# Optimization experiments

Measured on AMD Instinct MI355X. Metric: run time of the kernel, lower is better.

Reference implementation:

```python
import jax, jax.numpy as jnp
import numpy as np

N_NODES = 100000
N_EDGES = 1600000
N_GRAPHS = 2048


def _gcn_conv(x, src, dst, W, b, n_nodes):
    # PyG GCNConv: add self-loops, symmetric norm D^-1/2 A D^-1/2, then linear.
    h = x @ W  # [N, H]
    loop = jnp.arange(n_nodes, dtype=src.dtype)
    s = jnp.concatenate([src, loop])
    d = jnp.concatenate([dst, loop])
    deg = jax.ops.segment_sum(jnp.ones_like(d, dtype=h.dtype), d, num_segments=n_nodes)
    dinv = jax.lax.rsqrt(jnp.maximum(deg, 1.0))
    norm = dinv[s] * dinv[d]  # [E+N]
    msg = h[s] * norm[:, None]  # gathered, normalized messages
    out = jax.ops.segment_sum(msg, d, num_segments=n_nodes)
    return out + b


def _mean_pool(x, batch, n_graphs):
    sums = jax.ops.segment_sum(x, batch, num_segments=n_graphs)
    cnt = jax.ops.segment_sum(jnp.ones((x.shape[0],), x.dtype), batch, num_segments=n_graphs)
    return sums / jnp.maximum(cnt, 1.0)[:, None]


def setup_inputs() -> dict:
    key = jax.random.key(0)
    ks = jax.random.split(key, 8)
    x = jax.random.normal(ks[0], (N_NODES, 128), dtype=jnp.float32)
    edge_index = jax.random.randint(ks[1], (2, N_EDGES), 0, N_NODES, dtype=jnp.int64)
    batch = jnp.sort(jax.random.randint(ks[2], (N_NODES,), 0, N_GRAPHS, dtype=jnp.int64))
    W1 = jax.random.normal(ks[3], (128, 256), dtype=jnp.float32) * 0.05
    b1 = jnp.zeros((256,), jnp.float32)
    W2 = jax.random.normal(ks[4], (256, 256), dtype=jnp.float32) * 0.05
    b2 = jnp.zeros((256,), jnp.float32)
    Wc = jax.random.normal(ks[5], (256, 64), dtype=jnp.float32) * 0.05
    bc = jnp.zeros((64,), jnp.float32)
    return {"x": x, "edge_index": edge_index, "batch": batch,
            "W1": W1, "b1": b1, "W2": W2, "b2": b2, "Wc": Wc, "bc": bc}


def reference(x, edge_index, batch, W1, b1, W2, b2, Wc, bc):
    src, dst = edge_index[0], edge_index[1]
    n = x.shape[0]
    h = jax.nn.relu(_gcn_conv(x, src, dst, W1, b1, n))
    h = jax.nn.relu(_gcn_conv(h, src, dst, W2, b2, n))
    g = _mean_pool(h, batch, N_GRAPHS)  # [G, h2]
    logits = g @ Wc + bc
    return jax.nn.log_softmax(logits, axis=1)
```

## Files before the change

### kernel.cpp

```cpp
#include <hip/hip_runtime.h>
#include <hip/hip_bf16.h>

#define N_NODES 100000
#define N_EDGES 1600000
#define N_GRAPHS 2048
#define F0 128
#define F1 256
#define NCLS 64

#define BSHIFT 9
#define BNODES 512
#define NB 196
#define EPB 4096
#define NCHUNK 391
#define FLATN (NB * NCHUNK)

typedef unsigned int uint32;
typedef unsigned short u16;
typedef u16 u16x8 __attribute__((ext_vector_type(8)));
typedef __bf16 bf16x8 __attribute__((ext_vector_type(8)));
typedef float f32x4 __attribute__((ext_vector_type(4)));

__device__ __forceinline__ float blo(uint32 v) { return __builtin_bit_cast(float, v << 16); }
__device__ __forceinline__ float bhi(uint32 v) { return __builtin_bit_cast(float, v & 0xffff0000u); }
__device__ __forceinline__ float b16f(u16 v) { return __builtin_bit_cast(float, (uint32)v << 16); }
__device__ __forceinline__ u16 f2bf(float f) {
    uint32 u = __builtin_bit_cast(uint32, f);
    u += 0x7fffu + ((u >> 16) & 1u);
    return (u16)(u >> 16);
}
__device__ __forceinline__ uint32 pack2(float a, float b) {
    return (uint32)f2bf(a) | ((uint32)f2bf(b) << 16);
}
__device__ __forceinline__ float ub0(uint32 u) { return (float)(u & 255u); }
__device__ __forceinline__ float ub1(uint32 u) { return (float)((u >> 8) & 255u); }
__device__ __forceinline__ float ub2(uint32 u) { return (float)((u >> 16) & 255u); }
__device__ __forceinline__ float ub3(uint32 u) { return (float)(u >> 24); }

#define GLOAD_LDS16(g, l)                                                                  \
    __builtin_amdgcn_global_load_lds((const __attribute__((address_space(1))) void*)(g),   \
                                     (__attribute__((address_space(3))) void*)(l), 16, 0, 0)

#define SCAN_B 1024

__global__ void scan_partial(const int* __restrict__ in, int n, int* __restrict__ bsum) {
    __shared__ int lds[SCAN_B];
    int i = blockIdx.x * SCAN_B + threadIdx.x;
    lds[threadIdx.x] = (i < n) ? in[i] : 0;
    __syncthreads();
    for (int s = SCAN_B / 2; s > 0; s >>= 1) {
        if (threadIdx.x < s) lds[threadIdx.x] += lds[threadIdx.x + s];
        __syncthreads();
    }
    if (threadIdx.x == 0) bsum[blockIdx.x] = lds[0];
}

__global__ void scan_final(const int* __restrict__ in, int n, const int* __restrict__ bsum,
                           int nb, int* __restrict__ out) {
    __shared__ int lds[SCAN_B];
    __shared__ int bpre[128];
    if (threadIdx.x < 128) bpre[threadIdx.x] = (threadIdx.x < nb) ? bsum[threadIdx.x] : 0;
    __syncthreads();
    for (int s = 1; s < 128; s <<= 1) {
        int v = (threadIdx.x < 128 && threadIdx.x >= s) ? bpre[threadIdx.x - s] : 0;
        __syncthreads();
        if (threadIdx.x < 128) bpre[threadIdx.x] += v;
        __syncthreads();
    }
    int base = (blockIdx.x > 0) ? bpre[blockIdx.x - 1] : 0;
    int i = blockIdx.x * SCAN_B + threadIdx.x;
    int v = (i < n) ? in[i] : 0;
    lds[threadIdx.x] = v;
    __syncthreads();
    for (int s = 1; s < SCAN_B; s <<= 1) {
        int t = (threadIdx.x >= s) ? lds[threadIdx.x - s] : 0;
        __syncthreads();
        lds[threadIdx.x] += t;
        __syncthreads();
    }
    if (i < n) out[i + 1] = lds[threadIdx.x] + base;
    if (i == 0) out[0] = 0;
}


__global__ __launch_bounds__(256) void hist_pass(const int* __restrict__ dst,
                                                 int* __restrict__ hist) {
    __shared__ int lh[NB];
    int t = threadIdx.x, blk = blockIdx.x;
    if (t < NB) lh[t] = 0;
    __syncthreads();
#pragma unroll
    for (int k = 0; k < EPB / 256; ++k) {
        int e = blk * EPB + k * 256 + t;
        if (e < N_EDGES) atomicAdd(&lh[dst[e] >> BSHIFT], 1);
    }
    __syncthreads();
    if (t < NB) hist[t * NCHUNK + blk] = lh[t];
}

__global__ __launch_bounds__(256) void bin_pairs(const int* __restrict__ src,
                                                 const int* __restrict__ dst,
                                                 const int* __restrict__ histoff,
                                                 uint32* __restrict__ pairs) {
    __shared__ int lbase[NB];
    __shared__ int lcur[NB];
    int t = threadIdx.x, blk = blockIdx.x;
    if (t < NB) {
        lbase[t] = histoff[t * NCHUNK + blk];
        lcur[t] = 0;
    }
    __syncthreads();
#pragma unroll
    for (int k = 0; k < EPB / 256; ++k) {
        int e = blk * EPB + k * 256 + t;
        if (e < N_EDGES) {
            int d = dst[e], s = src[e];
            int b = d >> BSHIFT;
            int r = atomicAdd(&lcur[b], 1);
            pairs[lbase[b] + r] = (uint32)(d & (BNODES - 1)) | ((uint32)s << BSHIFT);
        }
    }
}

#define PCAP 16384

__global__ __launch_bounds__(256) void bucket_csr(const uint32* __restrict__ pairs,
                                                  const int* __restrict__ histoff,
                                                  int* __restrict__ offs,
                                                  int* __restrict__ csr,
                                                  float* __restrict__ dinv) {
    __shared__ uint32 lp[PCAP];
    __shared__ int lcnt[BNODES];
    __shared__ int lcur[BNODES];
    __shared__ int psum[256];
    int t = threadIdx.x, b = blockIdx.x;
    int n0 = b << BSHIFT;
    int nn = min(BNODES, N_NODES - n0);
    lcnt[t] = 0;
    lcnt[t + 256] = 0;
    __syncthreads();
    int ebase = histoff[b * NCHUNK];
    int eend = (b == NB - 1) ? N_EDGES : histoff[(b + 1) * NCHUNK];
    for (int i = ebase + t; i < eend; i += 256) {
        uint32 p = pairs[i];
        int li = i - ebase;
        if (li < PCAP) lp[li] = p;
        atomicAdd(&lcnt[p & (BNODES - 1)], 1);
    }
    __syncthreads();
    int c0 = lcnt[2 * t], c1 = lcnt[2 * t + 1];
    if (2 * t < nn) dinv[n0 + 2 * t] = rsqrtf((float)(c0 + 1));
    if (2 * t + 1 < nn) dinv[n0 + 2 * t + 1] = rsqrtf((float)(c1 + 1));
    psum[t] = c0 + c1;
    __syncthreads();
    for (int s = 1; s < 256; s <<= 1) {
        int v = (t >= s) ? psum[t - s] : 0;
        __syncthreads();
        psum[t] += v;
        __syncthreads();
    }
    int ep = psum[t] - (c0 + c1);
    lcur[2 * t] = ep;
    lcur[2 * t + 1] = ep + c0;
    if (2 * t < nn) offs[n0 + 2 * t] = ebase + ep;
    if (2 * t + 1 < nn) offs[n0 + 2 * t + 1] = ebase + ep + c0;
    if (b == NB - 1 && t == 0) offs[N_NODES] = N_EDGES;
    __syncthreads();
    for (int i = ebase + t; i < eend; i += 256) {
        int li = i - ebase;
        uint32 p = (li < PCAP) ? lp[li] : pairs[i];
        int r = atomicAdd(&lcur[p & (BNODES - 1)], 1);
        csr[ebase + r] = (int)(p >> BSHIFT);
    }
}


__global__ __launch_bounds__(256) void cast_q8_x(const float* __restrict__ x,
                                                 const float* __restrict__ dinv,
                                                 const int* __restrict__ batch,
                                                 u16* __restrict__ q8,
                                                 float* __restrict__ qs,
                                                 int* __restrict__ gcnt) {
    int node = blockIdx.x * 4 + (threadIdx.x >> 6);
    if (node >= N_NODES) return;
    int lane = threadIdx.x & 63;
    float d = dinv[node];
    float2 v = *(const float2*)&x[(size_t)node * F0 + lane * 2];
    float f0 = v.x * d, f1 = v.y * d;
    float m = fmaxf(fabsf(f0), fabsf(f1));
    for (int s = 32; s > 0; s >>= 1) m = fmaxf(m, __shfl_xor(m, s, 64));
    float inv = (m > 0.f) ? 127.f / m : 0.f;
    int u0 = (int)rintf(f0 * inv) + 128, u1 = (int)rintf(f1 * inv) + 128;
    q8[(size_t)node * 64 + lane] = (u16)((u0 & 255) | ((u1 & 255) << 8));
    if (lane == 0) {
        qs[node] = m * (1.f / 127.f);
        atomicAdd(&gcnt[batch[node]], 1);
    }
}


__global__ void transpose_w2(const float* __restrict__ W1, const float* __restrict__ W2,
                             u16* __restrict__ W1t, u16* __restrict__ W2t) {
    int id = blockIdx.x * blockDim.x + threadIdx.x;
    if (id < F0 * F1) {
        int k = id / F1, n = id % F1;
        W1t[(size_t)n * F0 + k] = f2bf(W1[id]);
    } else {
        int id2 = id - F0 * F1;
        if (id2 < F1 * F1) {
            int k = id2 / F1, n = id2 % F1;
            W2t[(size_t)n * F1 + k] = f2bf(W2[id2]);
        }
    }
}


template <int F>
__global__ __launch_bounds__(256) void aggregate_q8(const void* __restrict__ q8,
                                                    const float* __restrict__ qs,
                                                    const int* __restrict__ offs,
                                                    const int* __restrict__ csr,
                                                    const float* __restrict__ dinv,
                                                    u16* __restrict__ out) {
    constexpr int V = F / 64;
    int node = blockIdx.x * 4 + (threadIdx.x >> 6);
    if (node >= N_NODES) return;
    int lane = threadIdx.x & 63;
    float acc[V];
    float ssum;
    {
        float s = qs[node];
        ssum = s;
        if constexpr (V == 2) {
            uint32 q = (uint32)((const u16*)q8)[(size_t)node * 64 + lane];
            acc[0] = ub0(q) * s;
            acc[1] = ub1(q) * s;
        } else {
            uint32 q = ((const uint32*)q8)[(size_t)node * 64 + lane];
            acc[0] = ub0(q) * s;
            acc[1] = ub1(q) * s;
            acc[2] = ub2(q) * s;
            acc[3] = ub3(q) * s;
        }
    }
    int e0 = offs[node], e1 = offs[node + 1];
    for (int b = e0; b < e1; b += 64) {
        bool valid = (b + lane) < e1;
        int idx = valid ? csr[b + lane] : 0;
        float sv = valid ? qs[idx] : 0.f;
        int cnt = min(64, e1 - b);
        int t = 0;
        for (; t + 4 <= cnt; t += 4) {
            int j0 = __shfl(idx, t), j1 = __shfl(idx, t + 1);
            int j2 = __shfl(idx, t + 2), j3 = __shfl(idx, t + 3);
            float s0 = __shfl(sv, t), s1 = __shfl(sv, t + 1);
            float s2 = __shfl(sv, t + 2), s3 = __shfl(sv, t + 3);
            ssum += (s0 + s1) + (s2 + s3);
            if constexpr (V == 2) {
                uint32 a = (uint32)((const u16*)q8)[(size_t)j0 * 64 + lane];
                uint32 c = (uint32)((const u16*)q8)[(size_t)j1 * 64 + lane];
                uint32 d = (uint32)((const u16*)q8)[(size_t)j2 * 64 + lane];
                uint32 f = (uint32)((const u16*)q8)[(size_t)j3 * 64 + lane];
                acc[0] += ub0(a) * s0 + ub0(c) * s1 + ub0(d) * s2 + ub0(f) * s3;
                acc[1] += ub1(a) * s0 + ub1(c) * s1 + ub1(d) * s2 + ub1(f) * s3;
            } else {
                uint32 a = ((const uint32*)q8)[(size_t)j0 * 64 + lane];
                uint32 c = ((const uint32*)q8)[(size_t)j1 * 64 + lane];
                uint32 d = ((const uint32*)q8)[(size_t)j2 * 64 + lane];
                uint32 f = ((const uint32*)q8)[(size_t)j3 * 64 + lane];
                acc[0] += ub0(a) * s0 + ub0(c) * s1 + ub0(d) * s2 + ub0(f) * s3;
                acc[1] += ub1(a) * s0 + ub1(c) * s1 + ub1(d) * s2 + ub1(f) * s3;
                acc[2] += ub2(a) * s0 + ub2(c) * s1 + ub2(d) * s2 + ub2(f) * s3;
                acc[3] += ub3(a) * s0 + ub3(c) * s1 + ub3(d) * s2 + ub3(f) * s3;
            }
        }
        for (; t < cnt; ++t) {
            int j0 = __shfl(idx, t);
            float s0 = __shfl(sv, t);
            ssum += s0;
            if constexpr (V == 2) {
                uint32 a = (uint32)((const u16*)q8)[(size_t)j0 * 64 + lane];
                acc[0] += ub0(a) * s0;
                acc[1] += ub1(a) * s0;
            } else {
                uint32 a = ((const uint32*)q8)[(size_t)j0 * 64 + lane];
                acc[0] += ub0(a) * s0;
                acc[1] += ub1(a) * s0;
                acc[2] += ub2(a) * s0;
                acc[3] += ub3(a) * s0;
            }
        }
    }
    float di = dinv[node];
    float bias = 128.f * ssum;
    u16* orow = out + (size_t)node * F + lane * V;
    if constexpr (V == 2) {
        *(uint32*)orow = pack2((acc[0] - bias) * di, (acc[1] - bias) * di);
    } else {
        uint2 o;
        o.x = pack2((acc[0] - bias) * di, (acc[1] - bias) * di);
        o.y = pack2((acc[2] - bias) * di, (acc[3] - bias) * di);
        *(uint2*)orow = o;
    }
}


template <int K, bool QUANT>
__global__ __launch_bounds__(256) void gemm_fused(const u16* __restrict__ A,
                                                  const u16* __restrict__ Bt,
                                                  const float* __restrict__ bias,
                                                  const float* __restrict__ dinv,
                                                  int M,
                                                  uint32* __restrict__ q8,
                                                  float* __restrict__ qs,
                                                  const int* __restrict__ batch,
                                                  float* __restrict__ gpool) {
    constexpr int BM = 64, BN = 256, BK = 64;
    __shared__ __align__(16) char smem[40960];
    u16* As = (u16*)smem;
    u16* Bs = (u16*)smem + BM * BK;
    int tid = threadIdx.x;
    int lane = tid & 63;
    int wid = __builtin_amdgcn_readfirstlane(tid >> 6);
    int row0 = blockIdx.x * BM;
    int lr = lane & 15, lq = lane >> 4;
    int wn = wid * 64;
    int srow = lane >> 3;
    int schunk = (lane & 7) * 8;

    f32x4 acc[4][4];
#pragma unroll
    for (int i = 0; i < 4; ++i)
#pragma unroll
        for (int j = 0; j < 4; ++j) acc[i][j] = (f32x4){0.f, 0.f, 0.f, 0.f};

    for (int k0 = 0; k0 < K; k0 += BK) {
#pragma unroll
        for (int p = 0; p < 2; ++p) {
            int r0 = wid * 16 + p * 8;
            const u16* g = A + (size_t)(row0 + r0 + srow) * K + k0 + schunk;
            GLOAD_LDS16(g, As + r0 * BK);
        }
#pragma unroll
        for (int p = 0; p < 8; ++p) {
            int r0 = wid * 64 + p * 8;
            const u16* g = Bt + (size_t)(r0 + srow) * K + k0 + schunk;
            GLOAD_LDS16(g, Bs + r0 * BK);
        }
        __syncthreads();
#pragma unroll
        for (int kk = 0; kk < BK; kk += 32) {
            bf16x8 af[4], bfr[4];
#pragma unroll
            for (int i = 0; i < 4; ++i)
                af[i] = __builtin_bit_cast(bf16x8, *(const u16x8*)&As[(i * 16 + lr) * BK + kk + lq * 8]);
#pragma unroll
            for (int j = 0; j < 4; ++j)
                bfr[j] = __builtin_bit_cast(bf16x8, *(const u16x8*)&Bs[(wn + j * 16 + lr) * BK + kk + lq * 8]);
#pragma unroll
            for (int i = 0; i < 4; ++i)
#pragma unroll
                for (int j = 0; j < 4; ++j)
                    acc[i][j] = __builtin_amdgcn_mfma_f32_16x16x32_bf16(af[i], bfr[j], acc[i][j], 0, 0, 0);
        }
        __syncthreads();
    }

    u16(*P)[260] = (u16(*)[260])smem;
#pragma unroll
    for (int i = 0; i < 4; ++i) {
#pragma unroll
        for (int j = 0; j < 4; ++j) {
            int cl = wn + j * 16 + lr;
            float bv = bias[cl];
#pragma unroll
            for (int r = 0; r < 4; ++r) {
                int rl = i * 16 + lq * 4 + r;
                int row = row0 + rl;
                float v = 0.f;
                if (row < M) {
                    v = fmaxf(acc[i][j][r] + bv, 0.f);
                    if constexpr (QUANT) v *= dinv[row];
                }
                P[rl][cl] = f2bf(v);
            }
        }
    }

    if constexpr (QUANT) {
        float* rmax = (float*)(smem + 33280);
        __syncthreads();
        int row = tid & 63, q = tid >> 6;
        float m = 0.f;
#pragma unroll 8
        for (int i = 0; i < 64; ++i) m = fmaxf(m, b16f(P[row][q * 64 + i]));
        rmax[q * 64 + row] = m;
        __syncthreads();
        m = fmaxf(fmaxf(rmax[row], rmax[64 + row]), fmaxf(rmax[128 + row], rmax[192 + row]));
        int gr = row0 + row;
        if (gr < M) {
            float inv = (m > 0.f) ? 127.f / m : 0.f;
#pragma unroll
            for (int d = 0; d < 16; d += 4) {
                uint32 dw[4];
#pragma unroll
                for (int e = 0; e < 4; ++e) {
                    int cb = q * 64 + (d + e) * 4;
                    uint32 v0 = (uint32)((int)rintf(b16f(P[row][cb + 0]) * inv) + 128);
                    uint32 v1 = (uint32)((int)rintf(b16f(P[row][cb + 1]) * inv) + 128);
                    uint32 v2 = (uint32)((int)rintf(b16f(P[row][cb + 2]) * inv) + 128);
                    uint32 v3 = (uint32)((int)rintf(b16f(P[row][cb + 3]) * inv) + 128);
                    dw[e] = v0 | (v1 << 8) | (v2 << 16) | (v3 << 24);
                }
                *(uint4*)&q8[(size_t)gr * 64 + q * 16 + d] = make_uint4(dw[0], dw[1], dw[2], dw[3]);
            }
            if (q == 0) qs[gr] = m * (1.f / 127.f);
        }
    } else {
        int* batchl = (int*)(smem + 33280);
        if (tid < BM) {
            int row = row0 + tid;
            batchl[tid] = batch[row < M ? row : (M - 1)];
        }
        __syncthreads();
        int c = tid;
        int nrows = min(BM, M - row0);
        int cur = batchl[0];
        float sum = 0.f;
        for (int r = 0; r < nrows; ++r) {
            int gb = batchl[r];
            float v = b16f(P[r][c]);
            if (gb != cur) {
                atomicAdd(&gpool[(size_t)cur * BN + c], sum);
                sum = 0.f;
                cur = gb;
            }
            sum += v;
        }
        atomicAdd(&gpool[(size_t)cur * BN + c], sum);
    }
}


__global__ void classify(const float* __restrict__ gpool, const int* __restrict__ gcnt,
                         const float* __restrict__ Wc, const float* __restrict__ bc,
                         float* __restrict__ out) {
    int gr = blockIdx.x;
    int c = threadIdx.x;
    __shared__ float gl[F1];
    float inv = 1.f / fmaxf((float)gcnt[gr], 1.f);
    for (int k = c; k < F1; k += 64) gl[k] = gpool[(size_t)gr * F1 + k] * inv;
    __syncthreads();
    float acc = bc[c];
    for (int k = 0; k < F1; ++k) acc += gl[k] * Wc[k * NCLS + c];
    float m = acc;
    for (int s = 32; s > 0; s >>= 1) m = fmaxf(m, __shfl_xor(m, s, 64));
    float ex = __expf(acc - m);
    float sum = ex;
    for (int s = 32; s > 0; s >>= 1) sum += __shfl_xor(sum, s, 64);
    out[(size_t)gr * NCLS + c] = acc - m - __logf(sum);
}


extern "C" void kernel_launch(void* const* d_in, const int* in_sizes, int n_in,
                              void* d_out, int out_size, void* d_ws, size_t ws_size,
                              hipStream_t stream) {
    const float* x = (const float*)d_in[0];
    const int* ei = (const int*)d_in[1];
    const int* batch = (const int*)d_in[2];
    const float* W1 = (const float*)d_in[3];
    const float* b1 = (const float*)d_in[4];
    const float* W2 = (const float*)d_in[5];
    const float* b2 = (const float*)d_in[6];
    const float* Wc = (const float*)d_in[7];
    const float* bc = (const float*)d_in[8];
    float* out = (float*)d_out;
    const int* src = ei;
    const int* dst = ei + N_EDGES;

    char* w = (char*)d_ws;
    auto take = [&](size_t n) { char* p = w; w += (n + 255) & ~(size_t)255; return p; };
    float* dinv = (float*)take((size_t)N_NODES * 4);
    int* offs = (int*)take((size_t)(N_NODES + 1) * 4);
    int* hist = (int*)take((size_t)FLATN * 4);
    int* histoff = (int*)take((size_t)(FLATN + 1) * 4);
    int* bsum = (int*)take((size_t)1024 * 4);
    int* gcnt = (int*)take((size_t)N_GRAPHS * 4);
    uint32* pairs = (uint32*)take((size_t)N_EDGES * 4);
    int* csr = (int*)take((size_t)N_EDGES * 4);
    u16* q8x = (u16*)take((size_t)N_NODES * 64 * 2);
    float* qsx = (float*)take((size_t)N_NODES * 4);
    uint32* q8h = (uint32*)take((size_t)N_NODES * 64 * 4);
    float* qsh = (float*)take((size_t)N_NODES * 4);
    u16* aggx = (u16*)take((size_t)(N_NODES + 64) * F0 * 2);
    u16* agg1 = (u16*)take((size_t)(N_NODES + 64) * F1 * 2);
    u16* W1t = (u16*)take((size_t)F0 * F1 * 2);
    u16* W2t = (u16*)take((size_t)F1 * F1 * 2);
    float* gpool = (float*)take((size_t)N_GRAPHS * F1 * 4);

    hipMemsetAsync(gcnt, 0, (size_t)N_GRAPHS * 4, stream);
    hipMemsetAsync(gpool, 0, (size_t)N_GRAPHS * F1 * 4, stream);

    hist_pass<<<NCHUNK, 256, 0, stream>>>(dst, hist);
    {
        int nb = (FLATN + SCAN_B - 1) / SCAN_B;
        scan_partial<<<nb, SCAN_B, 0, stream>>>(hist, FLATN, bsum);
        scan_final<<<nb, SCAN_B, 0, stream>>>(hist, FLATN, bsum, nb, histoff);
    }
    bin_pairs<<<NCHUNK, 256, 0, stream>>>(src, dst, histoff, pairs);
    bucket_csr<<<NB, 256, 0, stream>>>(pairs, histoff, offs, csr, dinv);

    transpose_w2<<<(F0 * F1 + F1 * F1 + 255) / 256, 256, 0, stream>>>(W1, W2, W1t, W2t);
    cast_q8_x<<<(N_NODES + 3) / 4, 256, 0, stream>>>(x, dinv, batch, q8x, qsx, gcnt);

    int mblocks = (N_NODES + 63) / 64;

    aggregate_q8<F0><<<(N_NODES + 3) / 4, 256, 0, stream>>>(q8x, qsx, offs, csr, dinv, aggx);
    gemm_fused<F0, true><<<mblocks, 256, 0, stream>>>(aggx, W1t, b1, dinv, N_NODES,
                                                      q8h, qsh, nullptr, nullptr);

    aggregate_q8<F1><<<(N_NODES + 3) / 4, 256, 0, stream>>>(q8h, qsh, offs, csr, dinv, agg1);
    gemm_fused<F1, false><<<mblocks, 256, 0, stream>>>(agg1, W2t, b2, dinv, N_NODES,
                                                       nullptr, nullptr, batch, gpool);

    classify<<<N_GRAPHS, 64, 0, stream>>>(gpool, gcnt, Wc, bc, out);
}
```

Baseline: 427.6 us.

## Fuse neighbor aggregation into GEMM prologue, dropping intermediate aggregate buffers

The separate aggregate_q8 kernels are removed. Each GEMM block now gathers and normalizes the quantized neighbor rows for its 64 nodes straight into LDS, then runs the MFMA loop from that LDS tile, so the bf16 aggregate matrices are never written to or read back from global memory. The gather inner loop is also widened from 4 to 8 neighbors per step to keep more loads in flight. In exchange, LDS use per block grows to about 64KB for the 256-wide layer, which lowers occupancy. The latency-bound gather also now runs inside far fewer, larger blocks, and it cannot overlap with the GEMM phase.

```diff
diff --git a/kernel.cpp b/kernel.cpp
--- a/kernel.cpp
+++ b/kernel.cpp
@@ -215,17 +215,13 @@
 }
 
 
-template <int F>
-__global__ __launch_bounds__(256) void aggregate_q8(const void* __restrict__ q8,
-                                                    const float* __restrict__ qs,
-                                                    const int* __restrict__ offs,
-                                                    const int* __restrict__ csr,
-                                                    const float* __restrict__ dinv,
-                                                    u16* __restrict__ out) {
-    constexpr int V = F / 64;
-    int node = blockIdx.x * 4 + (threadIdx.x >> 6);
-    if (node >= N_NODES) return;
-    int lane = threadIdx.x & 63;
+template <int V>
+__device__ __forceinline__ void gather_node(const void* __restrict__ q8,
+                                            const float* __restrict__ qs,
+                                            const int* __restrict__ offs,
+                                            const int* __restrict__ csr,
+                                            const float* __restrict__ dinv,
+                                            int node, int lane, u16* __restrict__ dstrow) {
     float acc[V];
     float ssum;
     {
@@ -250,75 +246,81 @@
         float sv = valid ? qs[idx] : 0.f;
         int cnt = min(64, e1 - b);
         int t = 0;
-        for (; t + 4 <= cnt; t += 4) {
-            int j0 = __shfl(idx, t), j1 = __shfl(idx, t + 1);
-            int j2 = __shfl(idx, t + 2), j3 = __shfl(idx, t + 3);
-            float s0 = __shfl(sv, t), s1 = __shfl(sv, t + 1);
-            float s2 = __shfl(sv, t + 2), s3 = __shfl(sv, t + 3);
-            ssum += (s0 + s1) + (s2 + s3);
-            if constexpr (V == 2) {
-                uint32 a = (uint32)((const u16*)q8)[(size_t)j0 * 64 + lane];
-                uint32 c = (uint32)((const u16*)q8)[(size_t)j1 * 64 + lane];
-                uint32 d = (uint32)((const u16*)q8)[(size_t)j2 * 64 + lane];
-                uint32 f = (uint32)((const u16*)q8)[(size_t)j3 * 64 + lane];
-                acc[0] += ub0(a) * s0 + ub0(c) * s1 + ub0(d) * s2 + ub0(f) * s3;
-                acc[1] += ub1(a) * s0 + ub1(c) * s1 + ub1(d) * s2 + ub1(f) * s3;
-            } else {
-                uint32 a = ((const uint32*)q8)[(size_t)j0 * 64 + lane];
-                uint32 c = ((const uint32*)q8)[(size_t)j1 * 64 + lane];
-                uint32 d = ((const uint32*)q8)[(size_t)j2 * 64 + lane];
-                uint32 f = ((const uint32*)q8)[(size_t)j3 * 64 + lane];
-                acc[0] += ub0(a) * s0 + ub0(c) * s1 + ub0(d) * s2 + ub0(f) * s3;
-                acc[1] += ub1(a) * s0 + ub1(c) * s1 + ub1(d) * s2 + ub1(f) * s3;
-                acc[2] += ub2(a) * s0 + ub2(c) * s1 + ub2(d) * s2 + ub2(f) * s3;
-                acc[3] += ub3(a) * s0 + ub3(c) * s1 + ub3(d) * s2 + ub3(f) * s3;
+        for (; t + 8 <= cnt; t += 8) {
+            int j[8];
+            float s[8];
+#pragma unroll
+            for (int u = 0; u < 8; ++u) {
+                j[u] = __shfl(idx, t + u);
+                s[u] = __shfl(sv, t + u);
+            }
+            uint32 a[8];
+#pragma unroll
+            for (int u = 0; u < 8; ++u) {
+                if constexpr (V == 2)
+                    a[u] = (uint32)((const u16*)q8)[(size_t)j[u] * 64 + lane];
+                else
+                    a[u] = ((const uint32*)q8)[(size_t)j[u] * 64 + lane];
+            }
+#pragma unroll
+            for (int u = 0; u < 8; ++u) {
+                ssum += s[u];
+                acc[0] += ub0(a[u]) * s[u];
+                acc[1] += ub1(a[u]) * s[u];
+                if constexpr (V == 4) {
+                    acc[2] += ub2(a[u]) * s[u];
+                    acc[3] += ub3(a[u]) * s[u];
+                }
             }
         }
         for (; t < cnt; ++t) {
             int j0 = __shfl(idx, t);
             float s0 = __shfl(sv, t);
             ssum += s0;
-            if constexpr (V == 2) {
-                uint32 a = (uint32)((const u16*)q8)[(size_t)j0 * 64 + lane];
-                acc[0] += ub0(a) * s0;
-                acc[1] += ub1(a) * s0;
-            } else {
-                uint32 a = ((const uint32*)q8)[(size_t)j0 * 64 + lane];
-                acc[0] += ub0(a) * s0;
-                acc[1] += ub1(a) * s0;
+            uint32 a;
+            if constexpr (V == 2)
+                a = (uint32)((const u16*)q8)[(size_t)j0 * 64 + lane];
+            else
+                a = ((const uint32*)q8)[(size_t)j0 * 64 + lane];
+            acc[0] += ub0(a) * s0;
+            acc[1] += ub1(a) * s0;
+            if constexpr (V == 4) {
                 acc[2] += ub2(a) * s0;
                 acc[3] += ub3(a) * s0;
             }
         }
     }
     float di = dinv[node];
-    float bias = 128.f * ssum;
-    u16* orow = out + (size_t)node * F + lane * V;
+    float bb = 128.f * ssum;
     if constexpr (V == 2) {
-        *(uint32*)orow = pack2((acc[0] - bias) * di, (acc[1] - bias) * di);
+        *(uint32*)(dstrow + lane * 2) = pack2((acc[0] - bb) * di, (acc[1] - bb) * di);
     } else {
         uint2 o;
-        o.x = pack2((acc[0] - bias) * di, (acc[1] - bias) * di);
-        o.y = pack2((acc[2] - bias) * di, (acc[3] - bias) * di);
-        *(uint2*)orow = o;
+        o.x = pack2((acc[0] - bb) * di, (acc[1] - bb) * di);
+        o.y = pack2((acc[2] - bb) * di, (acc[3] - bb) * di);
+        *(uint2*)(dstrow + lane * 4) = o;
     }
 }
 
 
 template <int K, bool QUANT>
-__global__ __launch_bounds__(256) void gemm_fused(const u16* __restrict__ A,
-                                                  const u16* __restrict__ Bt,
-                                                  const float* __restrict__ bias,
-                                                  const float* __restrict__ dinv,
-                                                  int M,
-                                                  uint32* __restrict__ q8,
-                                                  float* __restrict__ qs,
-                                                  const int* __restrict__ batch,
-                                                  float* __restrict__ gpool) {
+__global__ __launch_bounds__(256) void gemm_agg(const void* __restrict__ q8src,
+                                                const float* __restrict__ qssrc,
+                                                const int* __restrict__ offs,
+                                                const int* __restrict__ csr,
+                                                const float* __restrict__ dinv,
+                                                const u16* __restrict__ Bt,
+                                                const float* __restrict__ bias,
+                                                int M,
+                                                uint32* __restrict__ q8out,
+                                                float* __restrict__ qsout,
+                                                const int* __restrict__ batch,
+                                                float* __restrict__ gpool) {
     constexpr int BM = 64, BN = 256, BK = 64;
-    __shared__ __align__(16) char smem[40960];
-    u16* As = (u16*)smem;
-    u16* Bs = (u16*)smem + BM * BK;
+    constexpr int ASZ = BM * K * 2;
+    __shared__ __align__(16) char smem[ASZ + 256 * BK * 2];
+    u16* Aagg = (u16*)smem;
+    u16* Bs = (u16*)(smem + ASZ);
     int tid = threadIdx.x;
     int lane = tid & 63;
     int wid = __builtin_amdgcn_readfirstlane(tid >> 6);
@@ -328,6 +330,21 @@
     int srow = lane >> 3;
     int schunk = (lane & 7) * 8;
 
+    for (int it = 0; it < 16; ++it) {
+        int rl = wid * 16 + it;
+        int node = row0 + rl;
+        u16* dstrow = Aagg + rl * K;
+        if (node < N_NODES) {
+            gather_node<K / 64>(q8src, qssrc, offs, csr, dinv, node, lane, dstrow);
+        } else {
+            if constexpr (K == 128)
+                *(uint32*)(dstrow + lane * 2) = 0;
+            else
+                *(uint2*)(dstrow + lane * 4) = make_uint2(0, 0);
+        }
+    }
+    __syncthreads();
+
     f32x4 acc[4][4];
 #pragma unroll
     for (int i = 0; i < 4; ++i)
@@ -335,12 +352,6 @@
         for (int j = 0; j < 4; ++j) acc[i][j] = (f32x4){0.f, 0.f, 0.f, 0.f};
 
     for (int k0 = 0; k0 < K; k0 += BK) {
-#pragma unroll
-        for (int p = 0; p < 2; ++p) {
-            int r0 = wid * 16 + p * 8;
-            const u16* g = A + (size_t)(row0 + r0 + srow) * K + k0 + schunk;
-            GLOAD_LDS16(g, As + r0 * BK);
-        }
 #pragma unroll
         for (int p = 0; p < 8; ++p) {
             int r0 = wid * 64 + p * 8;
@@ -353,10 +364,12 @@
             bf16x8 af[4], bfr[4];
 #pragma unroll
             for (int i = 0; i < 4; ++i)
-                af[i] = __builtin_bit_cast(bf16x8, *(const u16x8*)&As[(i * 16 + lr) * BK + kk + lq * 8]);
+                af[i] = __builtin_bit_cast(bf16x8,
+                                           *(const u16x8*)&Aagg[(i * 16 + lr) * K + k0 + kk + lq * 8]);
 #pragma unroll
             for (int j = 0; j < 4; ++j)
-                bfr[j] = __builtin_bit_cast(bf16x8, *(const u16x8*)&Bs[(wn + j * 16 + lr) * BK + kk + lq * 8]);
+                bfr[j] = __builtin_bit_cast(bf16x8,
+                                            *(const u16x8*)&Bs[(wn + j * 16 + lr) * BK + kk + lq * 8]);
 #pragma unroll
             for (int i = 0; i < 4; ++i)
 #pragma unroll
@@ -412,9 +425,9 @@
                     uint32 v3 = (uint32)((int)rintf(b16f(P[row][cb + 3]) * inv) + 128);
                     dw[e] = v0 | (v1 << 8) | (v2 << 16) | (v3 << 24);
                 }
-                *(uint4*)&q8[(size_t)gr * 64 + q * 16 + d] = make_uint4(dw[0], dw[1], dw[2], dw[3]);
-            }
-            if (q == 0) qs[gr] = m * (1.f / 127.f);
+                *(uint4*)&q8out[(size_t)gr * 64 + q * 16 + d] = make_uint4(dw[0], dw[1], dw[2], dw[3]);
+            }
+            if (q == 0) qsout[gr] = m * (1.f / 127.f);
         }
     } else {
         int* batchl = (int*)(smem + 33280);
@@ -492,8 +505,6 @@
     float* qsx = (float*)take((size_t)N_NODES * 4);
     uint32* q8h = (uint32*)take((size_t)N_NODES * 64 * 4);
     float* qsh = (float*)take((size_t)N_NODES * 4);
-    u16* aggx = (u16*)take((size_t)(N_NODES + 64) * F0 * 2);
-    u16* agg1 = (u16*)take((size_t)(N_NODES + 64) * F1 * 2);
     u16* W1t = (u16*)take((size_t)F0 * F1 * 2);
     u16* W2t = (u16*)take((size_t)F1 * F1 * 2);
     float* gpool = (float*)take((size_t)N_GRAPHS * F1 * 4);
@@ -515,13 +526,11 @@
 
     int mblocks = (N_NODES + 63) / 64;
 
-    aggregate_q8<F0><<<(N_NODES + 3) / 4, 256, 0, stream>>>(q8x, qsx, offs, csr, dinv, aggx);
-    gemm_fused<F0, true><<<mblocks, 256, 0, stream>>>(aggx, W1t, b1, dinv, N_NODES,
-                                                      q8h, qsh, nullptr, nullptr);
-
-    aggregate_q8<F1><<<(N_NODES + 3) / 4, 256, 0, stream>>>(q8h, qsh, offs, csr, dinv, agg1);
-    gemm_fused<F1, false><<<mblocks, 256, 0, stream>>>(agg1, W2t, b2, dinv, N_NODES,
-                                                       nullptr, nullptr, batch, gpool);
+    gemm_agg<F0, true><<<mblocks, 256, 0, stream>>>(q8x, qsx, offs, csr, dinv, W1t, b1,
+                                                    N_NODES, q8h, qsh, nullptr, nullptr);
+
+    gemm_agg<F1, false><<<mblocks, 256, 0, stream>>>(q8h, qsh, offs, csr, dinv, W2t, b2,
+                                                     N_NODES, nullptr, nullptr, batch, gpool);
 
     classify<<<N_GRAPHS, 64, 0, stream>>>(gpool, gcnt, Wc, bc, out);
 }
```

After: 626.6 us. +46.5%, slower.
